# Performance work log

Hardware: AMD Instinct MI355X
Metric: run time of the kernel (lower is better)

The kernel has to match this reference:

```python
import jax, jax.numpy as jnp
import numpy as np

N, C, H, W = 16, 128, 112, 112
P, HG, WG = 98, 16, 16  # 98 patches, 16x16 sample grid each


def setup_inputs() -> dict:
    key = jax.random.key(0)
    k1, k2 = jax.random.split(key)
    feature_maps = jax.random.normal(k1, (N, C, H, W), dtype=jnp.float32)
    # grid_sample normalized coords in [-1, 1]
    meshgrid = jax.random.uniform(k2, (N, P, HG, WG, 2), dtype=jnp.float32) * 2.0 - 1.0
    return {"feature_maps": feature_maps, "meshgrid": meshgrid}


def _grid_sample_bilinear_border(fm, grid):
    # fm: [N, C, H, W]; grid: [N, P, Hg, Wg, 2] (x, y) in [-1, 1]
    # torch grid_sample(mode='bilinear', padding_mode='border', align_corners=False)
    n, c, h, w = fm.shape
    gx, gy = grid[..., 0], grid[..., 1]
    # unnormalize (align_corners=False) then clamp to border
    x = jnp.clip((gx + 1.0) * (w * 0.5) - 0.5, 0.0, w - 1.0)
    y = jnp.clip((gy + 1.0) * (h * 0.5) - 0.5, 0.0, h - 1.0)
    x0 = jnp.floor(x)
    y0 = jnp.floor(y)
    wx = x - x0  # [N, P, Hg, Wg]
    wy = y - y0
    x0i = jnp.clip(x0.astype(jnp.int32), 0, w - 1)
    x1i = jnp.clip(x0i + 1, 0, w - 1)
    y0i = jnp.clip(y0.astype(jnp.int32), 0, h - 1)
    y1i = jnp.clip(y0i + 1, 0, h - 1)
    b = jnp.arange(n).reshape(n, 1, 1, 1)
    gather = lambda yi, xi: fm[b, :, yi, xi]  # -> [N, P, Hg, Wg, C]
    out = (gather(y0i, x0i) * ((1.0 - wy) * (1.0 - wx))[..., None]
           + gather(y0i, x1i) * ((1.0 - wy) * wx)[..., None]
           + gather(y1i, x0i) * (wy * (1.0 - wx))[..., None]
           + gather(y1i, x1i) * (wy * wx)[..., None])
    # [N, P, Hg, Wg, C] -> [N, P, C, Hg, Wg]
    return jnp.moveaxis(out, -1, 2)


def reference(feature_maps, meshgrid):
    # Single fused batched sample over all 98 patches (equivalent to the
    # torch loop of 98 grid_sample calls + stack + permute(1,0,2,3,4)).
    return _grid_sample_bilinear_border(feature_maps, meshgrid)
```

## Files before the change

### kernel.cpp

```cpp
#include <hip/hip_runtime.h>
#include <hip/hip_fp16.h>


#define NN 16
#define CC 128
#define HH 112
#define WW 112
#define PP 98
#define PTS 256
#define NPTS (PP * PTS)
#define HWs (HH * WW)
#define PAD 113
#define THREADS 512

typedef float f32x4 __attribute__((ext_vector_type(4)));
typedef unsigned int u32x4 __attribute__((ext_vector_type(4)));

__device__ __forceinline__ unsigned int pack2(float a, float b) {
  __half2 h = __floats2half2_rn(a, b);
  return *reinterpret_cast<unsigned int*>(&h);
}

__device__ __forceinline__ float2 unpack2(unsigned int q) {
  __half2 h = *reinterpret_cast<__half2*>(&q);
  return __half22float2(h);
}

__global__ __launch_bounds__(THREADS) void patches_kernel(
    const float* __restrict__ fm,
    const float* __restrict__ grid,
    float* __restrict__ out) {
  __shared__ unsigned int plane[HWs + PAD];

  const int cp = blockIdx.x;
  const int n = blockIdx.y;
  const int t = threadIdx.x;
  const int c0 = cp * 2;

  const f32x4* __restrict__ srcA =
      reinterpret_cast<const f32x4*>(fm + ((size_t)n * CC + c0) * HWs);
  const f32x4* __restrict__ srcB =
      reinterpret_cast<const f32x4*>(fm + ((size_t)n * CC + c0 + 1) * HWs);
  u32x4* dst = reinterpret_cast<u32x4*>(plane);
  for (int i = t; i < HWs / 4; i += THREADS) {
    const f32x4 a = __builtin_nontemporal_load(&srcA[i]);
    const f32x4 b = __builtin_nontemporal_load(&srcB[i]);
    u32x4 q;
    q.x = pack2(a.x, b.x);
    q.y = pack2(a.y, b.y);
    q.z = pack2(a.z, b.z);
    q.w = pack2(a.w, b.w);
    dst[i] = q;
  }
  if (t < PAD) plane[HWs + t] = 0u;
  __syncthreads();

  const float2* __restrict__ g =
      reinterpret_cast<const float2*>(grid) + (size_t)n * NPTS;
  float* __restrict__ obase = out + ((size_t)n * PP * CC + c0) * PTS;

#pragma unroll 7
  for (int it = 0; it < NPTS / THREADS; ++it) {
    const int pt = t + it * THREADS;
    const float2 gg = g[pt];

    const float x = fminf(fmaxf(fmaf(gg.x, (float)WW * 0.5f, (float)WW * 0.5f - 0.5f),
                                0.0f), (float)(WW - 1));
    const float y = fminf(fmaxf(fmaf(gg.y, (float)HH * 0.5f, (float)HH * 0.5f - 0.5f),
                                0.0f), (float)(HH - 1));
    const float x0f = floorf(x), y0f = floorf(y);
    const float wx = x - x0f, wy = y - y0f;

    const unsigned int* p0 = reinterpret_cast<const unsigned int*>(
        reinterpret_cast<const char*>(plane) + ((int)y0f * WW + (int)x0f) * 4);
    const float2 f00 = unpack2(p0[0]);
    const float2 f01 = unpack2(p0[1]);
    const float2 f10 = unpack2(p0[WW]);
    const float2 f11 = unpack2(p0[WW + 1]);

    const float ux = 1.0f - wx, uy = 1.0f - wy;
    const float w00 = uy * ux, w01 = uy * wx, w10 = wy * ux, w11 = wy * wx;

    float vA = f00.x * w00;
    vA = fmaf(f01.x, w01, vA);
    vA = fmaf(f10.x, w10, vA);
    vA = fmaf(f11.x, w11, vA);
    float vB = f00.y * w00;
    vB = fmaf(f01.y, w01, vB);
    vB = fmaf(f10.y, w10, vB);
    vB = fmaf(f11.y, w11, vB);

    float* o = obase + (size_t)(pt >> 8) * CC * PTS + (pt & 255);
    __builtin_nontemporal_store(vA, o);
    __builtin_nontemporal_store(vB, o + PTS);
  }
}

extern "C" void kernel_launch(void* const* d_in, const int* in_sizes, int n_in,
                              void* d_out, int out_size, void* d_ws, size_t ws_size,
                              hipStream_t stream) {
  const float* fm = (const float*)d_in[0];
  const float* grid = (const float*)d_in[1];
  float* out = (float*)d_out;

  dim3 grd(CC / 2, NN);
  dim3 blk(THREADS);
  patches_kernel<<<grd, blk, 0, stream>>>(fm, grid, out);
}
```

Before: 281.8 us.

## Process two channel pairs per block and vectorize grid loads and output stores

Each block now loops over two channel pairs, reusing the same LDS plane buffer with a barrier between them, so the grid is halved to 32x16 blocks. Each thread now handles four consecutive sample points per iteration, loading the grid coordinates as two float4 loads and writing 16-byte vector nontemporal stores instead of scalar stores. The aim is wider memory transactions and fewer, longer-lived blocks. The cost is less parallelism across the GPU, with 512 blocks instead of 1024, and the plane loads for the two channel pairs running one after the other with nothing overlapping them.

```diff
diff --git a/kernel.cpp b/kernel.cpp
--- a/kernel.cpp
+++ b/kernel.cpp
@@ -9,6 +9,7 @@
 #define PP 98
 #define PTS 256
 #define NPTS (PP * PTS)
+#define NQUADS (NPTS / 4)
 #define HWs (HH * WW)
 #define PAD 113
 #define THREADS 512
@@ -21,9 +22,30 @@
   return *reinterpret_cast<unsigned int*>(&h);
 }
 
-__device__ __forceinline__ float2 unpack2(unsigned int q) {
-  __half2 h = *reinterpret_cast<__half2*>(&q);
-  return __half22float2(h);
+__device__ __forceinline__ float2 samp(const unsigned int* __restrict__ plane,
+                                       float gx, float gy) {
+  const float x = fminf(fmaxf(fmaf(gx, (float)WW * 0.5f, (float)WW * 0.5f - 0.5f),
+                              0.0f), (float)(WW - 1));
+  const float y = fminf(fmaxf(fmaf(gy, (float)HH * 0.5f, (float)HH * 0.5f - 0.5f),
+                              0.0f), (float)(HH - 1));
+  const float x0f = floorf(x), y0f = floorf(y);
+  const float wx = x - x0f, wy = y - y0f;
+  const unsigned int* p0 = reinterpret_cast<const unsigned int*>(
+      reinterpret_cast<const char*>(plane) + ((int)y0f * WW + (int)x0f) * 4);
+  const __half2 h00 = *reinterpret_cast<const __half2*>(&p0[0]);
+  const __half2 h01 = *reinterpret_cast<const __half2*>(&p0[1]);
+  const __half2 h10 = *reinterpret_cast<const __half2*>(&p0[WW]);
+  const __half2 h11 = *reinterpret_cast<const __half2*>(&p0[WW + 1]);
+  const float2 f00 = __half22float2(h00);
+  const float2 f01 = __half22float2(h01);
+  const float2 f10 = __half22float2(h10);
+  const float2 f11 = __half22float2(h11);
+  const float ux = 1.0f - wx, uy = 1.0f - wy;
+  const float w00 = uy * ux, w01 = uy * wx, w10 = wy * ux, w11 = wy * wx;
+  float2 r;
+  r.x = fmaf(f11.x, w11, fmaf(f10.x, w10, fmaf(f01.x, w01, f00.x * w00)));
+  r.y = fmaf(f11.y, w11, fmaf(f10.y, w10, fmaf(f01.y, w01, f00.y * w00)));
+  return r;
 }
 
 __global__ __launch_bounds__(THREADS) void patches_kernel(
@@ -32,67 +54,57 @@
     float* __restrict__ out) {
   __shared__ unsigned int plane[HWs + PAD];
 
-  const int cp = blockIdx.x;
   const int n = blockIdx.y;
   const int t = threadIdx.x;
-  const int c0 = cp * 2;
+  const f32x4* __restrict__ g4 =
+      reinterpret_cast<const f32x4*>(grid + (size_t)n * NPTS * 2);
 
-  const f32x4* __restrict__ srcA =
-      reinterpret_cast<const f32x4*>(fm + ((size_t)n * CC + c0) * HWs);
-  const f32x4* __restrict__ srcB =
-      reinterpret_cast<const f32x4*>(fm + ((size_t)n * CC + c0 + 1) * HWs);
-  u32x4* dst = reinterpret_cast<u32x4*>(plane);
-  for (int i = t; i < HWs / 4; i += THREADS) {
-    const f32x4 a = __builtin_nontemporal_load(&srcA[i]);
-    const f32x4 b = __builtin_nontemporal_load(&srcB[i]);
-    u32x4 q;
-    q.x = pack2(a.x, b.x);
-    q.y = pack2(a.y, b.y);
-    q.z = pack2(a.z, b.z);
-    q.w = pack2(a.w, b.w);
-    dst[i] = q;
-  }
-  if (t < PAD) plane[HWs + t] = 0u;
-  __syncthreads();
+  for (int half = 0; half < 2; ++half) {
+    const int cp = blockIdx.x * 2 + half;
+    const int c0 = cp * 2;
 
-  const float2* __restrict__ g =
-      reinterpret_cast<const float2*>(grid) + (size_t)n * NPTS;
-  float* __restrict__ obase = out + ((size_t)n * PP * CC + c0) * PTS;
+    if (half) __syncthreads();
 
-#pragma unroll 7
-  for (int it = 0; it < NPTS / THREADS; ++it) {
-    const int pt = t + it * THREADS;
-    const float2 gg = g[pt];
+    const f32x4* __restrict__ srcA =
+        reinterpret_cast<const f32x4*>(fm + ((size_t)n * CC + c0) * HWs);
+    const f32x4* __restrict__ srcB =
+        reinterpret_cast<const f32x4*>(fm + ((size_t)n * CC + c0 + 1) * HWs);
+    u32x4* dst = reinterpret_cast<u32x4*>(plane);
+    for (int i = t; i < HWs / 4; i += THREADS) {
+      const f32x4 a = __builtin_nontemporal_load(&srcA[i]);
+      const f32x4 b = __builtin_nontemporal_load(&srcB[i]);
+      u32x4 q;
+      q.x = pack2(a.x, b.x);
+      q.y = pack2(a.y, b.y);
+      q.z = pack2(a.z, b.z);
+      q.w = pack2(a.w, b.w);
+      dst[i] = q;
+    }
+    if (t < PAD) plane[HWs + t] = 0u;
+    __syncthreads();
 
-    const float x = fminf(fmaxf(fmaf(gg.x, (float)WW * 0.5f, (float)WW * 0.5f - 0.5f),
-                                0.0f), (float)(WW - 1));
-    const float y = fminf(fmaxf(fmaf(gg.y, (float)HH * 0.5f, (float)HH * 0.5f - 0.5f),
-                                0.0f), (float)(HH - 1));
-    const float x0f = floorf(x), y0f = floorf(y);
-    const float wx = x - x0f, wy = y - y0f;
+    float* __restrict__ obase = out + ((size_t)n * PP * CC + c0) * PTS;
 
-    const unsigned int* p0 = reinterpret_cast<const unsigned int*>(
-        reinterpret_cast<const char*>(plane) + ((int)y0f * WW + (int)x0f) * 4);
-    const float2 f00 = unpack2(p0[0]);
-    const float2 f01 = unpack2(p0[1]);
-    const float2 f10 = unpack2(p0[WW]);
-    const float2 f11 = unpack2(p0[WW + 1]);
-
-    const float ux = 1.0f - wx, uy = 1.0f - wy;
-    const float w00 = uy * ux, w01 = uy * wx, w10 = wy * ux, w11 = wy * wx;
-
-    float vA = f00.x * w00;
-    vA = fmaf(f01.x, w01, vA);
-    vA = fmaf(f10.x, w10, vA);
-    vA = fmaf(f11.x, w11, vA);
-    float vB = f00.y * w00;
-    vB = fmaf(f01.y, w01, vB);
-    vB = fmaf(f10.y, w10, vB);
-    vB = fmaf(f11.y, w11, vB);
-
-    float* o = obase + (size_t)(pt >> 8) * CC * PTS + (pt & 255);
-    __builtin_nontemporal_store(vA, o);
-    __builtin_nontemporal_store(vB, o + PTS);
+#pragma unroll 2
+    for (int it = 0; it < 13; ++it) {
+      const int q = t + it * THREADS;
+      if (q < NQUADS) {
+        const f32x4 ga = g4[q * 2];
+        const f32x4 gb = g4[q * 2 + 1];
+        const float2 r0 = samp(plane, ga.x, ga.y);
+        const float2 r1 = samp(plane, ga.z, ga.w);
+        const float2 r2 = samp(plane, gb.x, gb.y);
+        const float2 r3 = samp(plane, gb.z, gb.w);
+        f32x4 vA, vB;
+        vA.x = r0.x; vA.y = r1.x; vA.z = r2.x; vA.w = r3.x;
+        vB.x = r0.y; vB.y = r1.y; vB.z = r2.y; vB.w = r3.y;
+        const int p = q >> 6;
+        const int s4 = (q & 63) * 4;
+        float* o = obase + (size_t)p * CC * PTS + s4;
+        __builtin_nontemporal_store(vA, reinterpret_cast<f32x4*>(o));
+        __builtin_nontemporal_store(vB, reinterpret_cast<f32x4*>(o + PTS));
+      }
+    }
   }
 }
 
@@ -103,7 +115,7 @@
   const float* grid = (const float*)d_in[1];
   float* out = (float*)d_out;
 
-  dim3 grd(CC / 2, NN);
+  dim3 grd(CC / 4, NN);
   dim3 blk(THREADS);
   patches_kernel<<<grd, blk, 0, stream>>>(fm, grid, out);
 }
```

Measured after the change: 283.2 us. Within noise of the previous version (+0.5%).
